# Kernel optimization log

Hardware: AMD Instinct MI355X
Metric: run time of the kernel (lower is better)

Reference implementation:

```python
import jax, jax.numpy as jnp
import numpy as np

STOKEN = 16
HEADS = 8


def _unfold(x):
    # torch Unfold(3): identity conv1d, pad 1 -> shifts [x[t-1], x[t], x[t+1]]
    # x: (B, C, M) -> (B, C, 3, M)
    z = jnp.zeros_like(x[:, :, :1])
    xm1 = jnp.concatenate([z, x[:, :, :-1]], axis=-1)
    xp1 = jnp.concatenate([x[:, :, 1:], z], axis=-1)
    return jnp.stack([xm1, x, xp1], axis=2)


def _fold(y):
    # torch Fold(3): identity conv_transpose1d, pad 1 (overlap-add adjoint of _unfold)
    # y: (..., 3, M) -> (..., M); out[s] = y[0, s+1] + y[1, s] + y[2, s-1]
    z0 = jnp.zeros_like(y[..., 0, :1])
    y0 = jnp.concatenate([y[..., 0, 1:], z0], axis=-1)
    y2 = jnp.concatenate([z0, y[..., 2, :-1]], axis=-1)
    return y0 + y[..., 1, :] + y2


def _refine_attention(sf, Wqkv, Wproj, bproj):
    # Attention over super-tokens; sf: (B, C, M)
    B, C, M = sf.shape
    hd = C // HEADS
    qkv = jnp.einsum('oc,bcm->bom', Wqkv, sf).reshape(B, HEADS, 3 * hd, M)
    q, k, v = qkv[:, :, :hd], qkv[:, :, hd:2 * hd], qkv[:, :, 2 * hd:]
    scale = hd ** -0.5
    attn = jnp.einsum('bhdm,bhdn->bhmn', k, q) * scale  # (B,H,M,M), softmax over query axis (faithful)
    attn = jax.nn.softmax(attn, axis=-1)
    out = jnp.einsum('bhdm,bhmn->bhdn', v, attn).reshape(B, C, M)
    return jnp.einsum('oc,bcm->bom', Wproj, out) + bproj[None, :, None]


def setup_inputs() -> dict:
    key = jax.random.key(0)
    k1, k2, k3 = jax.random.split(key, 3)
    B, N, C = 2, 32768, 256
    x = jax.random.normal(k1, (B, N, C), jnp.float32)
    Wqkv = jax.random.normal(k2, (3 * C, C), jnp.float32) * 0.02
    Wproj = jax.random.normal(k3, (C, C), jnp.float32) * 0.02
    bproj = jnp.zeros((C,), jnp.float32)
    return {'x': x, 'Wqkv': Wqkv, 'Wproj': Wproj, 'bproj': bproj}


def reference(x, Wqkv, Wproj, bproj):
    n = STOKEN
    B, N, C = x.shape  # N % n == 0, so no padding branch
    xc = jnp.transpose(x, (0, 2, 1))          # (B, C, N)
    m = N // n
    xw = xc.reshape(B, C, m, n)
    sf = xw.mean(-1)                           # adaptive_avg_pool1d -> (B, C, m)
    pix = jnp.transpose(xw, (0, 2, 3, 1))      # (B, m, n, C)
    scale = C ** -0.5
    # --- n_iter=1 affinity computation (torch.no_grad) ---
    sfu = jnp.transpose(_unfold(sf), (0, 3, 1, 2))             # (B, m, C, 3)
    aff = jax.nn.softmax(jnp.einsum('bmnc,bmck->bmnk', pix, sfu) * scale, axis=-1)
    aff = jax.lax.stop_gradient(aff)                            # (B, m, n, 3)
    aff_sum = _fold(jnp.transpose(aff.sum(2), (0, 2, 1)))       # (B, m)
    aff_sum = jax.lax.stop_gradient(aff_sum)
    # --- super-token features (scatter / overlap-add) ---
    sf2 = jnp.einsum('bmnc,bmnk->bmck', pix, aff)               # (B, m, C, 3)
    sf2 = _fold(jnp.transpose(sf2, (0, 2, 3, 1)))               # (B, C, m)
    sf2 = sf2 / (aff_sum[:, None, :] + 1e-12)
    # --- refine with small attention over super-tokens ---
    sf2 = _refine_attention(sf2, Wqkv, Wproj, bproj)            # (B, C, m)
    # --- broadcast back to pixels (gather) ---
    sfu2 = jnp.transpose(_unfold(sf2), (0, 3, 1, 2))            # (B, m, C, 3)
    pix2 = jnp.einsum('bmck,bmnk->bmcn', sfu2, aff)             # (B, m, C, n)
    out = jnp.transpose(pix2, (0, 2, 1, 3)).reshape(B, C, N)    # (B, C, N)
    return out
```

## Files before the change

kernel.cpp:

```cpp
#include <hip/hip_runtime.h>
#include <hip/hip_bf16.h>

#define BB 2
#define NN 32768
#define CC 256
#define SN 16
#define MM 2048
#define HH 8
#define HD 32
#define PP1 4
#define PPB 4
#define QSCALE 0.17677669529663687f
#define AFFSCALE 0.0625f

typedef unsigned short u16;
typedef __attribute__((ext_vector_type(8))) short bf16x8;
typedef __attribute__((ext_vector_type(4))) float f32x4;
typedef __attribute__((ext_vector_type(4))) unsigned short u16x4;

__device__ __forceinline__ u16 f2bfu(float x) {
    unsigned u = __float_as_uint(x);
    u = (u + 0x7fff + ((u >> 16) & 1)) >> 16;
    return (u16)u;
}

__global__ void k1_sf(const float* __restrict__ x, float* __restrict__ sf) {
    int blk = blockIdx.x;
    int b = blk / MM, j = blk % MM;
    int c = threadIdx.x;
    const float* xp = x + ((size_t)(b*NN + j*SN))*CC + c;
    float s = 0.f;
    #pragma unroll
    for (int i = 0; i < SN; ++i) s += xp[i*CC];
    sf[(size_t)blk*CC + c] = s * (1.0f/16.0f);
}

__global__ void k2p_aff(const float* __restrict__ x, const float* __restrict__ sf,
                        float* __restrict__ aff, float* __restrict__ P,
                        float* __restrict__ A) {
    int blk = blockIdx.x; int b = blk / MM, j = blk % MM;
    __shared__ float sfl[3][CC];
    __shared__ float xl[SN][CC];
    __shared__ float affl[SN][3];
    int tid = threadIdx.x;
    #pragma unroll
    for (int k = 0; k < 3; ++k) {
        int w = j + k - 1;
        sfl[k][tid] = (w >= 0 && w < MM) ? sf[((size_t)b*MM + w)*CC + tid] : 0.f;
    }
    for (int idx = tid; idx < SN*64; idx += 256) {
        int i = idx >> 6, c4 = (idx & 63) << 2;
        *(float4*)&xl[i][c4] = *(const float4*)&x[((size_t)(b*NN + j*SN + i))*CC + c4];
    }
    __syncthreads();
    int wave = tid >> 6, lane = tid & 63;
    for (int qi = 0; qi < 4; ++qi) {
        int i = wave*4 + qi;
        float d0=0.f, d1=0.f, d2=0.f;
        #pragma unroll
        for (int cq = 0; cq < 4; ++cq) {
            int c = lane + cq*64;
            float xv = xl[i][c];
            d0 += xv * sfl[0][c];
            d1 += xv * sfl[1][c];
            d2 += xv * sfl[2][c];
        }
        #pragma unroll
        for (int off = 32; off >= 1; off >>= 1) {
            d0 += __shfl_xor(d0, off, 64);
            d1 += __shfl_xor(d1, off, 64);
            d2 += __shfl_xor(d2, off, 64);
        }
        if (lane == 0) {
            float l0 = d0*AFFSCALE, l1 = d1*AFFSCALE, l2 = d2*AFFSCALE;
            float mx = fmaxf(l0, fmaxf(l1, l2));
            float e0 = __expf(l0-mx), e1 = __expf(l1-mx), e2 = __expf(l2-mx);
            float inv = 1.0f/(e0+e1+e2);
            float a0 = e0*inv, a1 = e1*inv, a2 = e2*inv;
            size_t base = ((size_t)blk*SN + i)*3;
            aff[base+0] = a0; aff[base+1] = a1; aff[base+2] = a2;
            affl[i][0] = a0; affl[i][1] = a1; affl[i][2] = a2;
        }
    }
    __syncthreads();
    {
        int c = tid;
        #pragma unroll
        for (int k = 0; k < 3; ++k) {
            float p = 0.f;
            #pragma unroll
            for (int i = 0; i < SN; ++i) p += xl[i][c] * affl[i][k];
            P[((size_t)blk*3 + k)*CC + c] = p;
        }
        if (tid < 3) {
            float a = 0.f;
            #pragma unroll
            for (int i = 0; i < SN; ++i) a += affl[i][tid];
            A[(size_t)blk*3 + tid] = a;
        }
    }
}

__global__ void k4a_mfma(const float* __restrict__ P, const float* __restrict__ A,
                         const float* __restrict__ wqkv,
                         u16* __restrict__ qh, u16* __restrict__ kh, u16* __restrict__ vth) {
    int mt = blockIdx.x, ot = blockIdx.y, b = blockIdx.z;
    int mm0 = mt*64, oo0 = ot*64;
    __shared__ u16 S[64][264];
    __shared__ u16 W[64][264];
    __shared__ float dn[64];
    int tid = threadIdx.x;
    if (tid < 64) {
        int m = mm0 + tid;
        float a0 = (m+1 < MM) ? A[((size_t)(b*MM + m+1))*3 + 0] : 0.f;
        float a1 =               A[((size_t)(b*MM + m  ))*3 + 1];
        float a2 = (m-1 >= 0)  ? A[((size_t)(b*MM + m-1))*3 + 2] : 0.f;
        dn[tid] = ((a0 + a1) + a2) + 1e-12f;
    }
    __syncthreads();
    const float* Pb = P + (size_t)b*MM*3*CC;
    for (int idx = tid; idx < 64*64; idx += 256) {
        int r = idx >> 6, c4 = (idx & 63) << 2;
        int m = mm0 + r;
        float4 p0 = make_float4(0.f,0.f,0.f,0.f), p2 = make_float4(0.f,0.f,0.f,0.f);
        if (m+1 < MM) p0 = *(const float4*)&Pb[((size_t)(m+1)*3 + 0)*CC + c4];
        float4 p1 = *(const float4*)&Pb[((size_t)m*3 + 1)*CC + c4];
        if (m-1 >= 0) p2 = *(const float4*)&Pb[((size_t)(m-1)*3 + 2)*CC + c4];
        float d = dn[r];
        float sx = ((p0.x+p1.x)+p2.x)/d, sy = ((p0.y+p1.y)+p2.y)/d;
        float sz = ((p0.z+p1.z)+p2.z)/d, sw = ((p0.w+p1.w)+p2.w)/d;
        *(u16x4*)&S[r][c4] = (u16x4){f2bfu(sx), f2bfu(sy), f2bfu(sz), f2bfu(sw)};
        float4 wv = *(const float4*)&wqkv[(size_t)(oo0 + r)*CC + c4];
        *(u16x4*)&W[r][c4] = (u16x4){f2bfu(wv.x), f2bfu(wv.y), f2bfu(wv.z), f2bfu(wv.w)};
    }
    __syncthreads();
    int w = tid >> 6, l = tid & 63;
    f32x4 acc[4] = {{0.f,0.f,0.f,0.f},{0.f,0.f,0.f,0.f},{0.f,0.f,0.f,0.f},{0.f,0.f,0.f,0.f}};
    #pragma unroll
    for (int kc = 0; kc < 8; ++kc) {
        bf16x8 bf = *(const bf16x8*)&W[w*16 + (l&15)][kc*32 + ((l>>4)<<3)];
        #pragma unroll
        for (int nt = 0; nt < 4; ++nt) {
            bf16x8 af = *(const bf16x8*)&S[nt*16 + (l&15)][kc*32 + ((l>>4)<<3)];
            acc[nt] = __builtin_amdgcn_mfma_f32_16x16x32_bf16(af, bf, acc[nt], 0, 0, 0);
        }
    }
    int o = oo0 + w*16 + (l&15);
    int h = o / 96, rr = o % 96;
    int bh = b*HH + h;
    int m0 = mm0 + ((l>>4)<<2);
    #pragma unroll
    for (int nt = 0; nt < 4; ++nt) {
        #pragma unroll
        for (int r = 0; r < 4; ++r) {
            int m = m0 + nt*16 + r;
            float v = acc[nt][r];
            if (rr < 32)      qh[((size_t)bh*MM + m)*HD + rr]       = f2bfu(v * QSCALE);
            else if (rr < 64) kh[((size_t)bh*MM + m)*HD + (rr-32)]  = f2bfu(v);
            else              vth[((size_t)bh*HD + (rr-64))*MM + m] = f2bfu(v);
        }
    }
}

__global__ void k4b_mfma(const u16* __restrict__ qh, const u16* __restrict__ kh,
                         float* __restrict__ ses) {
    int bx = blockIdx.x;
    int p = blockIdx.y;
    int bh = bx >> 5;
    int mt = bx & 31;
    int mm0 = mt * 64;
    int tid = threadIdx.x, w = tid >> 6, l = tid & 63;
    bf16x8 af = *(const bf16x8*)&kh[((size_t)bh*MM + mm0 + w*16 + (l&15))*HD + ((l>>4)<<3)];
    __shared__ u16 Qlds[64][40];
    float rs0=0.f, rs1=0.f, rs2=0.f, rs3=0.f;
    int nnbeg = p * (MM/PP1), nnend = nnbeg + (MM/PP1);
    for (int nn0 = nnbeg; nn0 < nnend; nn0 += 64) {
        __syncthreads();
        {
            int r = tid >> 2, ch = tid & 3;
            *(bf16x8*)&Qlds[r][ch*8] =
                *(const bf16x8*)&qh[((size_t)bh*MM + nn0 + r)*HD + ch*8];
        }
        __syncthreads();
        #pragma unroll
        for (int nt = 0; nt < 4; ++nt) {
            bf16x8 bf = *(const bf16x8*)&Qlds[nt*16 + (l&15)][(l>>4)<<3];
            f32x4 acc = {0.f,0.f,0.f,0.f};
            acc = __builtin_amdgcn_mfma_f32_16x16x32_bf16(af, bf, acc, 0, 0, 0);
            rs0 += __expf(acc[0]); rs1 += __expf(acc[1]);
            rs2 += __expf(acc[2]); rs3 += __expf(acc[3]);
        }
    }
    float rs[4] = {rs0, rs1, rs2, rs3};
    #pragma unroll
    for (int r = 0; r < 4; ++r) {
        float v = rs[r];
        v += __shfl_xor(v, 1, 64);
        v += __shfl_xor(v, 2, 64);
        v += __shfl_xor(v, 4, 64);
        v += __shfl_xor(v, 8, 64);
        if ((l & 15) == 0)
            ses[((size_t)p*BB*HH + bh)*MM + mm0 + w*16 + ((l>>4)<<2) + r] = v;
    }
}

__global__ void k4c_mfma(const u16* __restrict__ qh, const u16* __restrict__ kh,
                         const u16* __restrict__ vth, const float* __restrict__ ses,
                         float* __restrict__ part) {
    int bx = blockIdx.x;
    int p = blockIdx.y;
    int bh = bx >> 5;
    int ntile = bx & 31;
    int nn0 = ntile * 64;
    int b = bh >> 3, h = bh & 7;
    int tid = threadIdx.x, w = tid >> 6, l = tid & 63;
    bf16x8 qf[4];
    #pragma unroll
    for (int nt = 0; nt < 4; ++nt)
        qf[nt] = *(const bf16x8*)&qh[((size_t)bh*MM + nn0 + nt*16 + (l&15))*HD + ((l>>4)<<3)];
    __shared__ u16 Klds[64][40];
    __shared__ u16 Vtlds[32][72];
    __shared__ u16 Wlds[64][72];
    __shared__ float Rlds[64];
    f32x4 o0 = {0.f,0.f,0.f,0.f}, o1 = {0.f,0.f,0.f,0.f};
    int mmbeg = p * (MM/PPB), mmend = mmbeg + (MM/PPB);
    const size_t SESP = (size_t)BB*HH*MM;
    for (int mm0 = mmbeg; mm0 < mmend; mm0 += 64) {
        __syncthreads();
        {
            int r = tid >> 2, ch = tid & 3;
            *(bf16x8*)&Klds[r][ch*8] =
                *(const bf16x8*)&kh[((size_t)bh*MM + mm0 + r)*HD + ch*8];
            int d = tid >> 3, ch2 = tid & 7;
            *(bf16x8*)&Vtlds[d][ch2*8] =
                *(const bf16x8*)&vth[((size_t)bh*HD + d)*MM + mm0 + ch2*8];
            if (tid < 64) {
                size_t e = (size_t)bh*MM + mm0 + tid;
                float s = ses[e] + ses[SESP + e] + ses[2*SESP + e] + ses[3*SESP + e];
                Rlds[tid] = 1.0f / s;
            }
        }
        __syncthreads();
        {
            bf16x8 af = *(const bf16x8*)&Klds[w*16 + (l&15)][(l>>4)<<3];
            float ri[4];
            #pragma unroll
            for (int r = 0; r < 4; ++r) ri[r] = Rlds[w*16 + ((l>>4)<<2) + r];
            #pragma unroll
            for (int nt = 0; nt < 4; ++nt) {
                f32x4 s = {0.f,0.f,0.f,0.f};
                s = __builtin_amdgcn_mfma_f32_16x16x32_bf16(af, qf[nt], s, 0, 0, 0);
                unsigned p0 = (unsigned)f2bfu(__expf(s[0]) * ri[0])
                            | ((unsigned)f2bfu(__expf(s[1]) * ri[1]) << 16);
                unsigned p1 = (unsigned)f2bfu(__expf(s[2]) * ri[2])
                            | ((unsigned)f2bfu(__expf(s[3]) * ri[3]) << 16);
                uint2 pk; pk.x = p0; pk.y = p1;
                *(uint2*)&Wlds[nt*16 + (l&15)][w*16 + ((l>>4)<<2)] = pk;
            }
        }
        __syncthreads();
        #pragma unroll
        for (int ks = 0; ks < 2; ++ks) {
            bf16x8 a2 = *(const bf16x8*)&Wlds[w*16 + (l&15)][ks*32 + ((l>>4)<<3)];
            bf16x8 b20 = *(const bf16x8*)&Vtlds[(l&15)][ks*32 + ((l>>4)<<3)];
            bf16x8 b21 = *(const bf16x8*)&Vtlds[16 + (l&15)][ks*32 + ((l>>4)<<3)];
            o0 = __builtin_amdgcn_mfma_f32_16x16x32_bf16(a2, b20, o0, 0, 0, 0);
            o1 = __builtin_amdgcn_mfma_f32_16x16x32_bf16(a2, b21, o1, 0, 0, 0);
        }
    }
    int nnb = nn0 + w*16 + ((l>>4)<<2);
    int dcol = h*32 + (l&15);
    float* op = part + ((size_t)p*BB + b)*((size_t)MM*CC);
    #pragma unroll
    for (int r = 0; r < 4; ++r) {
        op[((size_t)nnb + r)*CC + dcol]      = o0[r];
        op[((size_t)nnb + r)*CC + dcol + 16] = o1[r];
    }
}

__global__ void k5_mfma(const float* __restrict__ part, const float* __restrict__ wproj,
                        const float* __restrict__ bproj, float* __restrict__ sf2r) {
    int mt = blockIdx.x, ot = blockIdx.y, b = blockIdx.z;
    int mm0 = mt*64, oo0 = ot*64;
    __shared__ u16 S[64][264];
    __shared__ u16 W[64][264];
    int tid = threadIdx.x;
    const size_t PARTP = (size_t)BB*MM*CC;
    const float* pb = part + (size_t)b*MM*CC;
    for (int idx = tid; idx < 64*64; idx += 256) {
        int r = idx >> 6, c4 = (idx & 63) << 2;
        size_t e = (size_t)(mm0 + r)*CC + c4;
        float4 s0 = *(const float4*)&pb[e];
        float4 s1 = *(const float4*)&pb[PARTP + e];
        float4 s2 = *(const float4*)&pb[2*PARTP + e];
        float4 s3 = *(const float4*)&pb[3*PARTP + e];
        float sx = s0.x+s1.x+s2.x+s3.x, sy = s0.y+s1.y+s2.y+s3.y;
        float sz = s0.z+s1.z+s2.z+s3.z, sw = s0.w+s1.w+s2.w+s3.w;
        *(u16x4*)&S[r][c4] = (u16x4){f2bfu(sx), f2bfu(sy), f2bfu(sz), f2bfu(sw)};
        float4 wv = *(const float4*)&wproj[(size_t)(oo0 + r)*CC + c4];
        *(u16x4*)&W[r][c4] = (u16x4){f2bfu(wv.x), f2bfu(wv.y), f2bfu(wv.z), f2bfu(wv.w)};
    }
    __syncthreads();
    int w = tid >> 6, l = tid & 63;
    f32x4 acc[4] = {{0.f,0.f,0.f,0.f},{0.f,0.f,0.f,0.f},{0.f,0.f,0.f,0.f},{0.f,0.f,0.f,0.f}};
    #pragma unroll
    for (int kc = 0; kc < 8; ++kc) {
        bf16x8 bf = *(const bf16x8*)&W[w*16 + (l&15)][kc*32 + ((l>>4)<<3)];
        #pragma unroll
        for (int nt = 0; nt < 4; ++nt) {
            bf16x8 af = *(const bf16x8*)&S[nt*16 + (l&15)][kc*32 + ((l>>4)<<3)];
            acc[nt] = __builtin_amdgcn_mfma_f32_16x16x32_bf16(af, bf, acc[nt], 0, 0, 0);
        }
    }
    int o = oo0 + w*16 + (l&15);
    float bp = bproj[o];
    int m0 = mm0 + ((l>>4)<<2);
    #pragma unroll
    for (int nt = 0; nt < 4; ++nt) {
        #pragma unroll
        for (int r = 0; r < 4; ++r) {
            sf2r[((size_t)b*CC + o)*MM + m0 + nt*16 + r] = acc[nt][r] + bp;
        }
    }
}

__global__ void k6_final(const float* __restrict__ sf2r, const float* __restrict__ aff,
                         float* __restrict__ out) {
    int jt = blockIdx.x, cq = blockIdx.y, b = blockIdx.z;
    int jb = jt*16, cq0 = cq*64;
    int tid = threadIdx.x;
    int jl = tid >> 4, il = tid & 15;
    int j = jb + jl;
    size_t abase = (((size_t)b*MM + j)*SN + il)*3;
    float a0 = aff[abase], a1 = aff[abase+1], a2 = aff[abase+2];
    __shared__ float stile[64][18];
    for (int idx = tid; idx < 64*18; idx += 256) {
        int cl = idx / 18, jo = idx % 18;
        int jj = jb - 1 + jo;
        stile[cl][jo] = (jj >= 0 && jj < MM) ? sf2r[((size_t)b*CC + cq0 + cl)*MM + jj] : 0.f;
    }
    __syncthreads();
    int t = jb*SN + tid;
    float* ob = out + (size_t)b*CC*NN + (size_t)cq0*NN + t;
    #pragma unroll 4
    for (int cl = 0; cl < 64; ++cl) {
        float v = stile[cl][jl]*a0 + stile[cl][jl+1]*a1 + stile[cl][jl+2]*a2;
        ob[(size_t)cl*NN] = v;
    }
}

extern "C" void kernel_launch(void* const* d_in, const int* in_sizes, int n_in,
                              void* d_out, int out_size, void* d_ws, size_t ws_size,
                              hipStream_t stream) {
    const float *x = nullptr, *wqkv = nullptr, *wproj = nullptr, *bproj = nullptr;
    for (int i = 0; i < n_in; ++i) {
        int sz = in_sizes[i];
        if (sz == BB*NN*CC)        x     = (const float*)d_in[i];
        else if (sz == 3*CC*CC)    wqkv  = (const float*)d_in[i];
        else if (sz == CC*CC)      wproj = (const float*)d_in[i];
        else if (sz == CC)         bproj = (const float*)d_in[i];
    }
    float* out = (float*)d_out;
    char* ws = (char*)d_ws;
    const size_t MB = 1024*1024;
    float* aff     = (float*)(ws);
    float* sfbuf   = (float*)(ws + 1*MB);
    u16*   qh      = (u16*)  (ws + 5*MB);
    u16*   kh      = (u16*)  (ws + 7*MB);
    u16*   vth     = (u16*)  (ws + 9*MB);
    float* ses     = (float*)(ws + 11*MB);
    float* A       = (float*)(ws + 11*MB + 512*1024);
    float* P       = (float*)(ws + 12*MB);
    float* part    = (float*)(ws + 12*MB);
    float* sf      = sfbuf;
    float* sf2r    = sfbuf;

    k1_sf   <<<BB*MM, 256, 0, stream>>>(x, sf);
    k2p_aff <<<BB*MM, 256, 0, stream>>>(x, sf, aff, P, A);
    k4a_mfma<<<dim3(MM/64, 12, BB), 256, 0, stream>>>(P, A, wqkv, qh, kh, vth);
    k4b_mfma<<<dim3(BB*HH*(MM/64), PP1), 256, 0, stream>>>(qh, kh, ses);
    k4c_mfma<<<dim3(BB*HH*(MM/64), PPB), 256, 0, stream>>>(qh, kh, vth, ses, part);
    k5_mfma <<<dim3(MM/64, 4, BB), 256, 0, stream>>>(part, wproj, bproj, sf2r);
    k6_final<<<dim3(MM/16, 4, BB), 256, 0, stream>>>(sf2r, aff, out);
}
```

Before: 127.4 us.

## Preload full Q slab in k4b and widen k4c query tile to 128

In the column-sum kernel, each block now loads its entire 512-row Q slab into shared memory once, so the loop over tiles runs with no barriers. The attention-output kernel now handles 128 query rows per block instead of 64. This halves the number of K/V tile reloads and the grid size, and doubles the MFMA work done per barrier. K fragments are read directly from global memory instead of being staged in LDS. The trade-offs are more LDS and register use per block and fewer blocks in flight, which may lower occupancy.

```diff
diff --git a/kernel.cpp b/kernel.cpp
--- a/kernel.cpp
+++ b/kernel.cpp
@@ -171,20 +171,19 @@
     int mm0 = mt * 64;
     int tid = threadIdx.x, w = tid >> 6, l = tid & 63;
     bf16x8 af = *(const bf16x8*)&kh[((size_t)bh*MM + mm0 + w*16 + (l&15))*HD + ((l>>4)<<3)];
-    __shared__ u16 Qlds[64][40];
+    __shared__ u16 Qlds[512][40];
+    int nnbeg = p * (MM/PP1);
+    for (int idx = tid; idx < 512*4; idx += 256) {
+        int r = idx >> 2, ch = idx & 3;
+        *(bf16x8*)&Qlds[r][ch*8] =
+            *(const bf16x8*)&qh[((size_t)bh*MM + nnbeg + r)*HD + ch*8];
+    }
+    __syncthreads();
     float rs0=0.f, rs1=0.f, rs2=0.f, rs3=0.f;
-    int nnbeg = p * (MM/PP1), nnend = nnbeg + (MM/PP1);
-    for (int nn0 = nnbeg; nn0 < nnend; nn0 += 64) {
-        __syncthreads();
-        {
-            int r = tid >> 2, ch = tid & 3;
-            *(bf16x8*)&Qlds[r][ch*8] =
-                *(const bf16x8*)&qh[((size_t)bh*MM + nn0 + r)*HD + ch*8];
-        }
-        __syncthreads();
+    for (int t = 0; t < 8; ++t) {
         #pragma unroll
         for (int nt = 0; nt < 4; ++nt) {
-            bf16x8 bf = *(const bf16x8*)&Qlds[nt*16 + (l&15)][(l>>4)<<3];
+            bf16x8 bf = *(const bf16x8*)&Qlds[t*64 + nt*16 + (l&15)][(l>>4)<<3];
             f32x4 acc = {0.f,0.f,0.f,0.f};
             acc = __builtin_amdgcn_mfma_f32_16x16x32_bf16(af, bf, acc, 0, 0, 0);
             rs0 += __expf(acc[0]); rs1 += __expf(acc[1]);
@@ -209,28 +208,25 @@
                          float* __restrict__ part) {
     int bx = blockIdx.x;
     int p = blockIdx.y;
-    int bh = bx >> 5;
-    int ntile = bx & 31;
-    int nn0 = ntile * 64;
+    int bh = bx >> 4;
+    int ntile = bx & 15;
+    int nn0 = ntile * 128;
     int b = bh >> 3, h = bh & 7;
     int tid = threadIdx.x, w = tid >> 6, l = tid & 63;
-    bf16x8 qf[4];
-    #pragma unroll
-    for (int nt = 0; nt < 4; ++nt)
+    bf16x8 qf[8];
+    #pragma unroll
+    for (int nt = 0; nt < 8; ++nt)
         qf[nt] = *(const bf16x8*)&qh[((size_t)bh*MM + nn0 + nt*16 + (l&15))*HD + ((l>>4)<<3)];
-    __shared__ u16 Klds[64][40];
     __shared__ u16 Vtlds[32][72];
-    __shared__ u16 Wlds[64][72];
+    __shared__ u16 Wlds[128][72];
     __shared__ float Rlds[64];
-    f32x4 o0 = {0.f,0.f,0.f,0.f}, o1 = {0.f,0.f,0.f,0.f};
+    f32x4 oa0 = {0.f,0.f,0.f,0.f}, oa1 = {0.f,0.f,0.f,0.f};
+    f32x4 ob0 = {0.f,0.f,0.f,0.f}, ob1 = {0.f,0.f,0.f,0.f};
     int mmbeg = p * (MM/PPB), mmend = mmbeg + (MM/PPB);
     const size_t SESP = (size_t)BB*HH*MM;
     for (int mm0 = mmbeg; mm0 < mmend; mm0 += 64) {
         __syncthreads();
         {
-            int r = tid >> 2, ch = tid & 3;
-            *(bf16x8*)&Klds[r][ch*8] =
-                *(const bf16x8*)&kh[((size_t)bh*MM + mm0 + r)*HD + ch*8];
             int d = tid >> 3, ch2 = tid & 7;
             *(bf16x8*)&Vtlds[d][ch2*8] =
                 *(const bf16x8*)&vth[((size_t)bh*HD + d)*MM + mm0 + ch2*8];
@@ -242,12 +238,12 @@
         }
         __syncthreads();
         {
-            bf16x8 af = *(const bf16x8*)&Klds[w*16 + (l&15)][(l>>4)<<3];
+            bf16x8 af = *(const bf16x8*)&kh[((size_t)bh*MM + mm0 + w*16 + (l&15))*HD + ((l>>4)<<3)];
             float ri[4];
             #pragma unroll
             for (int r = 0; r < 4; ++r) ri[r] = Rlds[w*16 + ((l>>4)<<2) + r];
             #pragma unroll
-            for (int nt = 0; nt < 4; ++nt) {
+            for (int nt = 0; nt < 8; ++nt) {
                 f32x4 s = {0.f,0.f,0.f,0.f};
                 s = __builtin_amdgcn_mfma_f32_16x16x32_bf16(af, qf[nt], s, 0, 0, 0);
                 unsigned p0 = (unsigned)f2bfu(__expf(s[0]) * ri[0])
@@ -261,20 +257,25 @@
         __syncthreads();
         #pragma unroll
         for (int ks = 0; ks < 2; ++ks) {
-            bf16x8 a2 = *(const bf16x8*)&Wlds[w*16 + (l&15)][ks*32 + ((l>>4)<<3)];
             bf16x8 b20 = *(const bf16x8*)&Vtlds[(l&15)][ks*32 + ((l>>4)<<3)];
             bf16x8 b21 = *(const bf16x8*)&Vtlds[16 + (l&15)][ks*32 + ((l>>4)<<3)];
-            o0 = __builtin_amdgcn_mfma_f32_16x16x32_bf16(a2, b20, o0, 0, 0, 0);
-            o1 = __builtin_amdgcn_mfma_f32_16x16x32_bf16(a2, b21, o1, 0, 0, 0);
-        }
-    }
-    int nnb = nn0 + w*16 + ((l>>4)<<2);
+            bf16x8 a2a = *(const bf16x8*)&Wlds[w*16 + (l&15)][ks*32 + ((l>>4)<<3)];
+            bf16x8 a2b = *(const bf16x8*)&Wlds[64 + w*16 + (l&15)][ks*32 + ((l>>4)<<3)];
+            oa0 = __builtin_amdgcn_mfma_f32_16x16x32_bf16(a2a, b20, oa0, 0, 0, 0);
+            oa1 = __builtin_amdgcn_mfma_f32_16x16x32_bf16(a2a, b21, oa1, 0, 0, 0);
+            ob0 = __builtin_amdgcn_mfma_f32_16x16x32_bf16(a2b, b20, ob0, 0, 0, 0);
+            ob1 = __builtin_amdgcn_mfma_f32_16x16x32_bf16(a2b, b21, ob1, 0, 0, 0);
+        }
+    }
+    int nna = nn0 + w*16 + ((l>>4)<<2);
     int dcol = h*32 + (l&15);
     float* op = part + ((size_t)p*BB + b)*((size_t)MM*CC);
     #pragma unroll
     for (int r = 0; r < 4; ++r) {
-        op[((size_t)nnb + r)*CC + dcol]      = o0[r];
-        op[((size_t)nnb + r)*CC + dcol + 16] = o1[r];
+        op[((size_t)nna + r)*CC + dcol]           = oa0[r];
+        op[((size_t)nna + r)*CC + dcol + 16]      = oa1[r];
+        op[((size_t)nna + 64 + r)*CC + dcol]      = ob0[r];
+        op[((size_t)nna + 64 + r)*CC + dcol + 16] = ob1[r];
     }
 }
 
@@ -379,7 +380,7 @@
     k2p_aff <<<BB*MM, 256, 0, stream>>>(x, sf, aff, P, A);
     k4a_mfma<<<dim3(MM/64, 12, BB), 256, 0, stream>>>(P, A, wqkv, qh, kh, vth);
     k4b_mfma<<<dim3(BB*HH*(MM/64), PP1), 256, 0, stream>>>(qh, kh, ses);
-    k4c_mfma<<<dim3(BB*HH*(MM/64), PPB), 256, 0, stream>>>(qh, kh, vth, ses, part);
+    k4c_mfma<<<dim3(BB*HH*(MM/128), PPB), 256, 0, stream>>>(qh, kh, vth, ses, part);
     k5_mfma <<<dim3(MM/64, 4, BB), 256, 0, stream>>>(part, wproj, bproj, sf2r);
     k6_final<<<dim3(MM/16, 4, BB), 256, 0, stream>>>(sf2r, aff, out);
 }
```

New measurement: 142.4 us. 1.12x slower.
